# Kernel tuning notes

Hardware: AMD Instinct MI355X
Metric: run time of the kernel (lower is better)

The kernel has to match this reference:

```python
import jax, jax.numpy as jnp
import numpy as np

B, P, F, E, H, V = 128, 196, 2048, 512, 1024, 10000
TMAX = 30  # max(captions_len) - 1 decode steps
BN_EPS = 1e-5


def setup_inputs() -> dict:
    key = jax.random.key(0)
    ks = jax.random.split(key, 14)
    encoder_feat = jax.random.normal(ks[0], (B, P, F), jnp.float32)
    gt_captions = jax.random.randint(ks[1], (B, TMAX + 1), 0, V, dtype=jnp.int32)
    lens = jax.random.randint(ks[2], (B,), 2, TMAX + 2, dtype=jnp.int32)
    lens = lens.at[0].set(TMAX + 1)
    captions_len = jnp.sort(lens)[::-1]  # sorted descending, as the torch slicing assumes
    embedding = jax.random.uniform(ks[3], (V, E), jnp.float32, -0.1, 0.1)
    W_init = jax.random.normal(ks[4], (E, F), jnp.float32) * np.sqrt(2.0 / F)
    b_init = jnp.zeros((E,), jnp.float32)
    bn_gamma = jnp.ones((E,), jnp.float32)
    bn_beta = jnp.zeros((E,), jnp.float32)
    s = 1.0 / np.sqrt(H)
    W_ih = jax.random.uniform(ks[5], (4 * H, E), jnp.float32, -s, s)
    b_ih = jax.random.uniform(ks[6], (4 * H,), jnp.float32, -s, s)
    W_hh = jax.random.uniform(ks[7], (4 * H, H), jnp.float32, -s, s)
    b_hh = jax.random.uniform(ks[8], (4 * H,), jnp.float32, -s, s)
    W_fc = jax.random.normal(ks[9], (V, H), jnp.float32) * np.sqrt(2.0 / H)
    b_fc = jnp.zeros((V,), jnp.float32)
    return {
        'encoder_feat': encoder_feat, 'gt_captions': gt_captions, 'captions_len': captions_len,
        'embedding': embedding, 'W_init': W_init, 'b_init': b_init,
        'bn_gamma': bn_gamma, 'bn_beta': bn_beta,
        'W_ih': W_ih, 'b_ih': b_ih, 'W_hh': W_hh, 'b_hh': b_hh,
        'W_fc': W_fc, 'b_fc': b_fc,
    }


def _lstm_cell(h, c, x, W_ih, b_ih, W_hh, b_hh):
    # PyTorch LSTMCell: gates = x W_ih^T + b_ih + h W_hh^T + b_hh, order [i, f, g, o]
    gates = x @ W_ih.T + b_ih + h @ W_hh.T + b_hh
    i, f, g, o = jnp.split(gates, 4, axis=-1)
    c_new = jax.nn.sigmoid(f) * c + jax.nn.sigmoid(i) * jnp.tanh(g)
    h_new = jax.nn.sigmoid(o) * jnp.tanh(c_new)
    return h_new, c_new


def reference(encoder_feat, gt_captions, captions_len, embedding, W_init, b_init,
              bn_gamma, bn_beta, W_ih, b_ih, W_hh, b_hh, W_fc, b_fc):
    batch = encoder_feat.shape[0]
    hidden = W_hh.shape[1]
    # t == 0: image feature -> sigmoid(linear) -> BatchNorm1d (eval: rm=0, rv=1)
    feat = encoder_feat.mean(axis=1)                      # [B, F]
    x0 = jax.nn.sigmoid(feat @ W_init.T + b_init)         # [B, E]
    x0 = bn_gamma * (x0 / jnp.sqrt(1.0 + BN_EPS)) + bn_beta
    h0 = jnp.zeros((batch, hidden), x0.dtype)
    c0 = jnp.zeros((batch, hidden), x0.dtype)
    h, c = _lstm_cell(h0, c0, x0, W_ih, b_ih, W_hh, b_hh)
    # decode steps t = 1..TMAX over ground-truth token embeddings
    emb = embedding[gt_captions[:, :TMAX]]                # [B, T, E]
    xs = jnp.swapaxes(emb, 0, 1)                          # [T, B, E]

    def step(carry, x_t):
        h, c = carry
        h, c = _lstm_cell(h, c, x_t, W_ih, b_ih, W_hh, b_hh)
        preds = h @ W_fc.T + b_fc                         # [B, V]
        return (h, c), preds

    _, preds = jax.lax.scan(step, (h, c), xs)             # [T, B, V]
    preds = jnp.swapaxes(preds, 0, 1)                     # [B, T, V]
    # rows beyond batch_size_t were never written in torch (zeros tensor) -> mask
    mask = jnp.arange(TMAX)[None, :] < (captions_len - 1)[:, None]  # [B, T]
    return jnp.where(mask[:, :, None], preds, 0.0)
```

## Files before the change

### kernel.cpp

```cpp
#include <hip/hip_runtime.h>
#include <math.h>

typedef __bf16 bf16;
typedef __bf16 bf16x8 __attribute__((ext_vector_type(8)));
typedef __bf16 bf16x4 __attribute__((ext_vector_type(4)));
typedef float f32x4 __attribute__((ext_vector_type(4)));

#define MFMA_B16(a,b,c) __builtin_amdgcn_mfma_f32_16x16x32_bf16((a),(b),(c),0,0,0)

constexpr int TMAXc = 30;
constexpr int Bc = 128, Pc = 196, Fc = 2048, Ec = 512, Hc = 1024, Vc = 10000;
constexpr int G4c = 4 * Hc;
constexpr int NSTEP = TMAXc + 1;
constexpr int MALLc = NSTEP * Bc;
constexpr int MOUTc = TMAXc * Bc;
constexpr int NBLK = 256;

__device__ __forceinline__ float fsigm(float x){
  return __fdividef(1.0f, 1.0f + __expf(-x));
}
__device__ __forceinline__ float ftanh(float x){
  return 1.0f - __fdividef(2.0f, __expf(2.0f*x) + 1.0f);
}
__device__ __forceinline__ float sel4(float a, float b, float c, float d, int i){
  float x = (i & 1) ? b : a;
  float y = (i & 1) ? d : c;
  return (i & 2) ? y : x;
}

__device__ __forceinline__ void gll16(const void* g, void* l){
  __builtin_amdgcn_global_load_lds((const __attribute__((address_space(1))) void*)g,
                                   (__attribute__((address_space(3))) void*)l, 16, 0, 0);
}

__device__ __forceinline__ void wt16(bf16* p, bf16x8 v){
  asm volatile("global_store_dwordx4 %0, %1, off sc0 sc1" :: "v"(p), "v"(v) : "memory");
}

__device__ __forceinline__ int aldf(int* f){
  return __hip_atomic_load(f, __ATOMIC_RELAXED, __HIP_MEMORY_SCOPE_AGENT);
}

__device__ __forceinline__ void waitflag(int* f, int tgt){
  long long t0 = __builtin_amdgcn_s_memrealtime();
  while (aldf(f) < tgt) {
    __builtin_amdgcn_s_sleep(1);
    if (__builtin_amdgcn_s_memrealtime() - t0 > 100000) break;
  }
}

__device__ __forceinline__ void waitflags4(int* F, int& f1, int& f2, int& f3){
  long long t0 = __builtin_amdgcn_s_memrealtime();
  for (;;) {
    int f0 = aldf(F + 0);
    f1 = aldf(F + 1);
    f2 = aldf(F + 2);
    f3 = aldf(F + 3);
    if (f0 >= 32) break;
    __builtin_amdgcn_s_sleep(1);
    if (__builtin_amdgcn_s_memrealtime() - t0 > 100000) break;
  }
}


__global__ void mean_kernel(const float* __restrict__ enc, bf16* __restrict__ feat){
  int blk = blockIdx.x, b = blk >> 1, half = blk & 1;
  int f0 = half*1024 + threadIdx.x*4;
  const float* p = enc + (size_t)b*Pc*Fc + f0;
  float4 s = {0.f,0.f,0.f,0.f};
  #pragma unroll 4
  for (int q = 0; q < Pc; ++q) {
    float4 v = *(const float4*)(p + (size_t)q*Fc);
    s.x += v.x; s.y += v.y; s.z += v.z; s.w += v.w;
  }
  const float r = 1.0f/(float)Pc;
  bf16x4 o = { (bf16)(s.x*r), (bf16)(s.y*r), (bf16)(s.z*r), (bf16)(s.w*r) };
  *(bf16x4*)&feat[b*Fc + f0] = o;
}

__global__ void conv_kernel(const float* __restrict__ src, bf16* __restrict__ dst, int n4){
  int i = blockIdx.x*256 + threadIdx.x;
  if (i >= n4) return;
  float4 v = ((const float4*)src)[i];
  bf16x4 o = { (bf16)v.x, (bf16)v.y, (bf16)v.z, (bf16)v.w };
  *(bf16x4*)&dst[i*4] = o;
}

__global__ void permconv_ih(const float* __restrict__ W, bf16* __restrict__ Wp){
  int i = blockIdx.x*256 + threadIdx.x;
  if (i >= G4c*Ec/4) return;
  int i4 = i*4;
  int rp = i4 >> 9, k = i4 & 511;
  int g = rp & 3, j = rp >> 2;
  float4 v = *(const float4*)&W[(size_t)(g*Hc + j)*Ec + k];
  bf16x4 o = { (bf16)v.x, (bf16)v.y, (bf16)v.z, (bf16)v.w };
  *(bf16x4*)&Wp[i4] = o;
}

__global__ void permsplit_hh(const float* __restrict__ W, bf16* __restrict__ Whi, bf16* __restrict__ Wlo){
  int i = blockIdx.x*256 + threadIdx.x;
  if (i >= G4c*Hc/4) return;
  int i4 = i*4;
  int rp = i4 >> 10, k = i4 & 1023;
  int g = rp & 3, j = rp >> 2;
  float4 v = *(const float4*)&W[(size_t)(g*Hc + j)*Hc + k];
  bf16 h0=(bf16)v.x, h1=(bf16)v.y, h2=(bf16)v.z, h3=(bf16)v.w;
  bf16x4 hi = { h0, h1, h2, h3 };
  bf16x4 lo = { (bf16)(v.x-(float)h0), (bf16)(v.y-(float)h1), (bf16)(v.z-(float)h2), (bf16)(v.w-(float)h3) };
  *(bf16x4*)&Whi[i4] = hi;
  *(bf16x4*)&Wlo[i4] = lo;
}

__global__ void split_kernel(const float* __restrict__ W, bf16* __restrict__ Whi, bf16* __restrict__ Wlo, int n4){
  int i = blockIdx.x*256 + threadIdx.x;
  if (i >= n4) return;
  float4 v = ((const float4*)W)[i];
  bf16 h0=(bf16)v.x, h1=(bf16)v.y, h2=(bf16)v.z, h3=(bf16)v.w;
  bf16x4 hi = { h0, h1, h2, h3 };
  bf16x4 lo = { (bf16)(v.x-(float)h0), (bf16)(v.y-(float)h1), (bf16)(v.z-(float)h2), (bf16)(v.w-(float)h3) };
  *(bf16x4*)&Whi[i*4] = hi;
  *(bf16x4*)&Wlo[i*4] = lo;
}

__global__ void bcomb_kernel(const float* __restrict__ bih, const float* __restrict__ bhh, float* __restrict__ bc){
  int i = blockIdx.x*256 + threadIdx.x;
  if (i >= G4c) return;
  int g = i & 3, j = i >> 2;
  bc[i] = bih[g*Hc + j] + bhh[g*Hc + j];
}

__global__ void gather_kernel(const float* __restrict__ emb, const int* __restrict__ gt, bf16* __restrict__ X){
  int idx = blockIdx.x*256 + threadIdx.x;
  if (idx >= MOUTc*(Ec/4)) return;
  int r = idx >> 7, ei = (idx & 127) * 4;
  int s = (r >> 7) + 1, b = r & 127;
  int tok = gt[b*(TMAXc+1) + (s-1)];
  float4 v = *(const float4*)(emb + (size_t)tok*Ec + ei);
  bf16x4 o = { (bf16)v.x, (bf16)v.y, (bf16)v.z, (bf16)v.w };
  *(bf16x4*)&X[(size_t)(s*Bc + b)*Ec + ei] = o;
}

__global__ void build_ridx(const int* __restrict__ lens, int* __restrict__ meta){
  int i = blockIdx.x*256 + threadIdx.x;
  if (i >= MOUTc) return;
  int t = i >> 7, b = i & 127;
  int S = 0, R = 0;
  for (int bb = 0; bb < 128; ++bb) {
    int l = lens[bb] - 1;
    S += (t < l) ? t : l;
    R += l;
  }
  if (i == 0) meta[0] = R;
  if (i >= R) meta[1 + i] = 0;
  if (t < lens[b] - 1) meta[1 + S + b] = i;
}

__global__ void zerofill(const int* __restrict__ lens, float* __restrict__ out){
  int i = blockIdx.x*256 + threadIdx.x;
  if (i >= MOUTc*2500) return;
  int row = i / 2500, c4 = i - row*2500;
  int b = row / TMAXc, t = row - b*TMAXc;
  if (t >= lens[b] - 1) {
    float4 z = {0.f,0.f,0.f,0.f};
    *(float4*)(out + (size_t)row*Vc + c4*4) = z;
  }
}

__global__ __launch_bounds__(256, 2) void initA(
  const bf16* __restrict__ feat, const bf16* __restrict__ Wi, float* __restrict__ part)
{
  __shared__ alignas(16) bf16 sA[128*32], sB[128*32];
  int tid = threadIdx.x, lane = tid & 63, w = tid >> 6, wr = w >> 1, wc = w & 1;
  int nt = blockIdx.x & 3, kc = blockIdx.x >> 2;
  int n0 = nt*128;

  f32x4 acc[4][4] = {};
  for (int kt = kc*256; kt < kc*256 + 256; kt += 32) {
    #pragma unroll
    for (int is = 0; is < 2; ++is) {
      int p = tid*16 + is*4096;
      int r = p >> 6, c = (p & 63) >> 1;
      int ldsoff = w*512 + is*2048;
      gll16(feat + (size_t)r*Fc + kt + c, &sA[ldsoff]);
      gll16(Wi + (size_t)(n0 + r)*Fc + kt + c, &sB[ldsoff]);
    }
    __syncthreads();
    int koff = (lane >> 4) * 8;
    bf16x8 ah[4], bh[4];
    #pragma unroll
    for (int mi = 0; mi < 4; ++mi)
      ah[mi] = *(const bf16x8*)&sA[(wr*64 + mi*16 + (lane & 15))*32 + koff];
    #pragma unroll
    for (int ni = 0; ni < 4; ++ni)
      bh[ni] = *(const bf16x8*)&sB[(wc*64 + ni*16 + (lane & 15))*32 + koff];
    #pragma unroll
    for (int mi = 0; mi < 4; ++mi)
      #pragma unroll
      for (int ni = 0; ni < 4; ++ni)
        acc[mi][ni] = MFMA_B16(ah[mi], bh[ni], acc[mi][ni]);
    __syncthreads();
  }
  #pragma unroll
  for (int mi = 0; mi < 4; ++mi)
    #pragma unroll
    for (int ni = 0; ni < 4; ++ni) {
      int lrow = wr*64 + mi*16 + ((lane >> 4) << 2);
      int col = n0 + wc*64 + ni*16 + (lane & 15);
      #pragma unroll
      for (int j = 0; j < 4; ++j)
        part[((size_t)kc*128 + lrow + j)*512 + col] = acc[mi][ni][j];
    }
}

__global__ void initB(const float* __restrict__ part, const float* __restrict__ binit,
                      const float* __restrict__ gam, const float* __restrict__ bet,
                      bf16* __restrict__ Xall)
{
  int i = blockIdx.x*256 + threadIdx.x;
  if (i >= 128*512) return;
  int col = i & 511;
  float v = 0.f;
  #pragma unroll
  for (int kc = 0; kc < 8; ++kc) v += part[(size_t)kc*128*512 + i];
  const float rbn = rsqrtf(1.0f + 1e-5f);
  v = fsigm(v + binit[col]);
  v = gam[col]*(v*rbn) + bet[col];
  Xall[i] = (bf16)v;
}

template<int EPI, bool SPLIT, bool XSWZ>
__global__ __launch_bounds__(256, 2) void gemm_kernel(
  const bf16* __restrict__ Ahi, const bf16* __restrict__ Alo,
  const bf16* __restrict__ Bhi, const bf16* __restrict__ Blo,
  int M, int N, int K, int mtiles,
  const float* __restrict__ p0,
  bf16* __restrict__ outb, float* __restrict__ outf, const int* __restrict__ meta)
{
  constexpr int BK = 32;
  __shared__ alignas(16) bf16 sAh[128*BK], sBh[128*BK];
  __shared__ alignas(16) bf16 sAl[SPLIT ? 128*BK : 8], sBl[SPLIT ? 128*BK : 8];

  int tid = threadIdx.x;
  int lane = tid & 63, w = tid >> 6, wr = w >> 1, wc = w & 1;
  int bid = blockIdx.x;
  if constexpr (XSWZ) {
    int nwg = gridDim.x, q = nwg >> 3, r = nwg & 7;
    int x = bid & 7, o = bid >> 3;
    bid = (x < r ? x*(q+1) : r*(q+1) + (x-r)*q) + o;
  }
  int nt = bid / mtiles, mt = bid - nt*mtiles;
  int m0 = mt*128, n0 = nt*128;

  int R = M;
  if constexpr (EPI == 2) {
    R = meta[0];
    if (m0 >= R) return;
  }

  int sr = (tid*16) >> 6;
  int gr0, gr1;
  if constexpr (EPI == 2) { gr0 = meta[1 + m0 + sr]; gr1 = meta[1 + m0 + sr + 64]; }
  else                    { gr0 = m0 + sr;           gr1 = m0 + sr + 64; }

  f32x4 acc[4][4] = {};

  for (int kt = 0; kt < K; kt += BK) {
    #pragma unroll
    for (int is = 0; is < 2; ++is) {
      int p = tid*16 + is*4096;
      int r = p >> 6, c = (p & 63) >> 1;
      int ldsoff = w*512 + is*2048;
      int ga = is ? gr1 : gr0;
      gll16(Ahi + (size_t)ga*K + kt + c, &sAh[ldsoff]);
      int rb = n0 + r; rb = rb < N ? rb : N - 1;
      gll16(Bhi + (size_t)rb*K + kt + c, &sBh[ldsoff]);
      if constexpr (SPLIT) {
        gll16(Alo + (size_t)ga*K + kt + c, &sAl[ldsoff]);
        gll16(Blo + (size_t)rb*K + kt + c, &sBl[ldsoff]);
      }
    }
    __syncthreads();

    int koff = (lane >> 4) * 8;
    bf16x8 ah[4], bh[4], al[SPLIT?4:1], bl[SPLIT?4:1];
    #pragma unroll
    for (int mi = 0; mi < 4; ++mi) {
      int rr = wr*64 + mi*16 + (lane & 15);
      ah[mi] = *(const bf16x8*)&sAh[rr*BK + koff];
      if constexpr (SPLIT) al[mi] = *(const bf16x8*)&sAl[rr*BK + koff];
    }
    #pragma unroll
    for (int ni = 0; ni < 4; ++ni) {
      int rr = wc*64 + ni*16 + (lane & 15);
      bh[ni] = *(const bf16x8*)&sBh[rr*BK + koff];
      if constexpr (SPLIT) bl[ni] = *(const bf16x8*)&sBl[rr*BK + koff];
    }
    #pragma unroll
    for (int mi = 0; mi < 4; ++mi)
      #pragma unroll
      for (int ni = 0; ni < 4; ++ni) {
        acc[mi][ni] = MFMA_B16(ah[mi], bh[ni], acc[mi][ni]);
        if constexpr (SPLIT) {
          acc[mi][ni] = MFMA_B16(ah[mi], bl[ni], acc[mi][ni]);
          acc[mi][ni] = MFMA_B16(al[mi], bh[ni], acc[mi][ni]);
        }
      }
    __syncthreads();
  }

  #pragma unroll
  for (int mi = 0; mi < 4; ++mi) {
    #pragma unroll
    for (int ni = 0; ni < 4; ++ni) {
      int lrow = m0 + wr*64 + mi*16 + ((lane >> 4) << 2);
      int col = n0 + wc*64 + ni*16 + (lane & 15);
      #pragma unroll
      for (int j = 0; j < 4; ++j) {
        int rr = lrow + j;
        float v = acc[mi][ni][j];
        if constexpr (EPI == 1) {
          outb[(size_t)rr*G4c + col] = (bf16)(v + p0[col]);
        } else {
          if (rr < R && col < N) {
            int val = meta[1 + rr];
            int t = val >> 7, b = val & 127;
            outf[(size_t)b*(TMAXc*Vc) + (size_t)t*Vc + col] = v + p0[col];
          }
        }
      }
    }
  }
}


__global__ __launch_bounds__(256, 1) void lstm_persist(
  const bf16* __restrict__ Whi, const bf16* __restrict__ Wlo,
  const bf16* __restrict__ Xg,
  bf16* __restrict__ hCh, bf16* __restrict__ hCl,
  bf16* __restrict__ Hh, bf16* __restrict__ Hl,
  const int* __restrict__ lens,
  int* __restrict__ flg)
{
  extern __shared__ char sWc[];
  int tid = threadIdx.x, lane = tid & 63, w = tid >> 6;
  int bid = blockIdx.x;
  int strip = bid >> 1, rh = bid & 1;
  int pc0 = strip * 32;
  int row0 = rh * 64 + w * 16;
  int grp = strip >> 5;
  char* scr = sWc + 131072 + w*512;

  for (int ch = tid; ch < 4096; ch += 256) {
    int p = ch >> 7;
    int k = (ch & 127) * 8;
    int ni = p >> 4, bp = p & 15;
    int ks = k >> 5, kg = (k >> 3) & 3;
    int off = (((ks*2 + ni)*4 + kg)*16 + bp) * 16;
    bf16x8 vh = *(const bf16x8*)&Whi[(size_t)(pc0 + p)*Hc + k];
    bf16x8 vl = *(const bf16x8*)&Wlo[(size_t)(pc0 + p)*Hc + k];
    *(bf16x8*)(sWc + off) = vh;
    *(bf16x8*)(sWc + 65536 + off) = vl;
  }
  __syncthreads();

  int bp = lane & 15;
  int bk = (lane >> 4) << 3;
  int rbase = row0 + ((lane >> 4) << 2);
  int e = lane & 3;
  const char* sWhiB = sWc + lane*16;
  const char* sWloB = sWc + 65536 + lane*16;

  int Lh = lens[rh * 64];
  if (Lh > NSTEP) Lh = NSTEP;
  int lenv = lens[row0 + (lane & 15)] - 1;

  float creg[2] = {0.f, 0.f};
  float xgv[2][4];
  #pragma unroll
  for (int ni = 0; ni < 2; ++ni)
    #pragma unroll
    for (int j = 0; j < 4; ++j)
      xgv[ni][j] = (float)Xg[(size_t)(rbase + j)*G4c + pc0 + ni*16 + bp];

#define GATEQ(g, fg) do { if (s > 0) { \
    if (tid == 0 && (fg) < 32) waitflag(&flg[(s*2 + rh)*4 + (g)], 32); \
    __builtin_amdgcn_s_barrier(); \
    asm volatile("" ::: "memory"); } } while (0)

#define LOADQ(qh, ql, g) do { \
    _Pragma("unroll") \
    for (int i = 0; i < 8; ++i) { \
      qh[i] = *(const bf16x8*)(pah + ((g)*8 + i)*32); \
      ql[i] = *(const bf16x8*)(pal + ((g)*8 + i)*32); \
    } \
    asm volatile("" ::: "memory"); } while (0)

#define MFMAQ(qh, ql, g) do { \
    _Pragma("unroll") \
    for (int i = 0; i < 8; ++i) { \
      int ks = (g)*8 + i; \
      _Pragma("unroll") \
      for (int ni = 0; ni < 2; ++ni) { \
        bf16x8 bvh = *(const bf16x8*)(sWhiB + (ks*2 + ni)*1024); \
        bf16x8 bvl = *(const bf16x8*)(sWloB + (ks*2 + ni)*1024); \
        aHH[ni] = MFMA_B16(qh[i], bvh, aHH[ni]); \
        aHL[ni] = MFMA_B16(qh[i], bvl, aHL[ni]); \
        aLH[ni] = MFMA_B16(ql[i], bvh, aLH[ni]); \
      } \
    } } while (0)

  #pragma unroll 1
  for (int s = 0; s < Lh; ++s) {
    const bf16* pah = hCh + (size_t)s*Bc*Hc + (size_t)(row0 + bp)*Hc + bk;
    const bf16* pal = hCl + (size_t)s*Bc*Hc + (size_t)(row0 + bp)*Hc + bk;
    bf16* hwh = hCh + (size_t)(s+1)*Bc*Hc;
    bf16* hwl = hCl + (size_t)(s+1)*Bc*Hc;

    f32x4 aHH[2], aHL[2], aLH[2];
    #pragma unroll
    for (int ni = 0; ni < 2; ++ni) {
      #pragma unroll
      for (int j = 0; j < 4; ++j) aHH[ni][j] = xgv[ni][j];
      aHL[ni] = (f32x4){0.f,0.f,0.f,0.f};
      aLH[ni] = (f32x4){0.f,0.f,0.f,0.f};
    }

    bf16x8 qh0[8], ql0[8], qh1[8], ql1[8];
    int f1 = 32, f2 = 32, f3 = 32;

    if (s > 0) {
      if (tid == 0) waitflags4(&flg[(s*2 + rh)*4], f1, f2, f3);
      __builtin_amdgcn_s_barrier();
      asm volatile("" ::: "memory");
    }
    LOADQ(qh0, ql0, 0);
    GATEQ(1, f1); LOADQ(qh1, ql1, 1);
    MFMAQ(qh0, ql0, 0);
    GATEQ(2, f2); LOADQ(qh0, ql0, 2);
    MFMAQ(qh1, ql1, 1);
    GATEQ(3, f3); LOADQ(qh1, ql1, 3);
    MFMAQ(qh0, ql0, 2);
    MFMAQ(qh1, ql1, 3);

    #pragma unroll
    for (int ni = 0; ni < 2; ++ni) {
      float v0 = aHH[ni][0] + aHL[ni][0] + aLH[ni][0];
      float v1 = aHH[ni][1] + aHL[ni][1] + aLH[ni][1];
      float v2 = aHH[ni][2] + aHL[ni][2] + aLH[ni][2];
      float v3 = aHH[ni][3] + aHL[ni][3] + aLH[ni][3];
      float g0 = sel4(v0, v1, v2, v3, e);
      float g1 = __shfl_xor(sel4(v0, v1, v2, v3, e ^ 1), 1);
      float g2 = __shfl_xor(sel4(v0, v1, v2, v3, e ^ 2), 2);
      float g3 = __shfl_xor(sel4(v0, v1, v2, v3, e ^ 3), 3);
      float gI = sel4(g0, g1, g2, g3, e);
      float gF = sel4(g0, g1, g2, g3, e ^ 1);
      float gG = sel4(g0, g1, g2, g3, e ^ 2);
      float gO = sel4(g0, g1, g2, g3, e ^ 3);

      float co = creg[ni];
      float cn = fsigm(gF)*co + fsigm(gI)*ftanh(gG);
      float hn = fsigm(gO)*ftanh(cn);
      creg[ni] = cn;
      bf16 hhi = (bf16)hn;
      int r16 = ((lane >> 4) << 2) + e;
      int c8  = ni*4 + (bp >> 2);
      *(bf16*)(scr + (r16*8 + c8)*2) = hhi;
      *(bf16*)(scr + 256 + (r16*8 + c8)*2) = (bf16)(hn - (float)hhi);
    }

    asm volatile("s_waitcnt lgkmcnt(0)" ::: "memory");
    __builtin_amdgcn_sched_barrier(0);

    if (lane < 32) {
      int r = lane & 15, buf = lane >> 4;
      bf16x8 vv = *(const bf16x8*)(scr + buf*256 + r*16);
      bf16* dst = (buf ? hwl : hwh) + (size_t)(row0 + r)*Hc + strip*8;
      wt16(dst, vv);
    }

    __syncthreads();
    if (tid == 0 && s + 1 < Lh)
      __hip_atomic_fetch_add(&flg[((s+1)*2 + rh)*4 + grp], 1,
                             __ATOMIC_RELAXED, __HIP_MEMORY_SCOPE_AGENT);

    if (s > 0 && lane >= 32 && (s - 1) < lenv) {
      int r = lane & 15, buf = (lane >> 4) & 1;
      bf16x8 vv = *(const bf16x8*)(scr + buf*256 + r*16);
      *(bf16x8*)((buf ? Hl : Hh) + (size_t)((s-1)*Bc + row0 + r)*Hc + strip*8) = vv;
    }
    if (s + 1 < Lh) {
      #pragma unroll
      for (int ni = 0; ni < 2; ++ni)
        #pragma unroll
        for (int j = 0; j < 4; ++j)
          xgv[ni][j] = (float)Xg[(size_t)((s+1)*Bc + rbase + j)*G4c + pc0 + ni*16 + bp];
    }
  }
#undef GATEQ
#undef LOADQ
#undef MFMAQ
}


extern "C" void kernel_launch(void* const* d_in, const int* in_sizes, int n_in,
                              void* d_out, int out_size, void* d_ws, size_t ws_size,
                              hipStream_t stream)
{
  const float* enc   = (const float*)d_in[0];
  const int*   gt    = (const int*)  d_in[1];
  const int*   lens  = (const int*)  d_in[2];
  const float* emb   = (const float*)d_in[3];
  const float* Winit = (const float*)d_in[4];
  const float* binit = (const float*)d_in[5];
  const float* gam   = (const float*)d_in[6];
  const float* bet   = (const float*)d_in[7];
  const float* Wih   = (const float*)d_in[8];
  const float* bih   = (const float*)d_in[9];
  const float* Whh   = (const float*)d_in[10];
  const float* bhh   = (const float*)d_in[11];
  const float* Wfc   = (const float*)d_in[12];
  const float* bfc   = (const float*)d_in[13];
  float* out = (float*)d_out;

  char* ws = (char*)d_ws;
  size_t off = 0;
  auto alloc = [&](size_t bytes) -> char* {
    char* p = ws + off;
    off += (bytes + 255) & ~(size_t)255;
    return p;
  };

  bf16* featB  = (bf16*)alloc((size_t)Bc*Fc*2);
  bf16* WinitB = (bf16*)alloc((size_t)Ec*Fc*2);
  bf16* WihpB  = (bf16*)alloc((size_t)G4c*Ec*2);
  bf16* WhhHi  = (bf16*)alloc((size_t)G4c*Hc*2);
  bf16* WhhLo  = (bf16*)alloc((size_t)G4c*Hc*2);
  bf16* WfcHi  = (bf16*)alloc((size_t)Vc*Hc*2);
  bf16* WfcLo  = (bf16*)alloc((size_t)Vc*Hc*2);
  float* bcomb = (float*)alloc((size_t)G4c*4);
  bf16* Xall   = (bf16*)alloc((size_t)MALLc*Ec*2);
  bf16* Xg     = (bf16*)alloc((size_t)MALLc*G4c*2);
  bf16* hChH   = (bf16*)alloc((size_t)(NSTEP+1)*Bc*Hc*2);
  bf16* hChL   = (bf16*)alloc((size_t)(NSTEP+1)*Bc*Hc*2);
  bf16* HallH  = (bf16*)alloc((size_t)MOUTc*Hc*2);
  bf16* HallL  = (bf16*)alloc((size_t)MOUTc*Hc*2);
  float* part  = (float*)alloc((size_t)8*128*512*4);
  int*  meta   = (int*) alloc((size_t)(1 + MOUTc)*4);
  int*  flg    = (int*) alloc((size_t)256*4);

  if (off > ws_size) return;

  hipMemsetAsync(hChH, 0, (size_t)Bc*Hc*2, stream);
  hipMemsetAsync(hChL, 0, (size_t)Bc*Hc*2, stream);
  hipMemsetAsync(flg, 0, (size_t)256*4, stream);

  mean_kernel<<<256, 256, 0, stream>>>(enc, featB);
  conv_kernel<<<(Ec*Fc/4 + 255)/256, 256, 0, stream>>>(Winit, WinitB, Ec*Fc/4);
  permconv_ih<<<(G4c*Ec/4 + 255)/256, 256, 0, stream>>>(Wih, WihpB);
  permsplit_hh<<<(G4c*Hc/4 + 255)/256, 256, 0, stream>>>(Whh, WhhHi, WhhLo);
  split_kernel<<<(Vc*Hc/4 + 255)/256, 256, 0, stream>>>(Wfc, WfcHi, WfcLo, Vc*Hc/4);
  bcomb_kernel<<<(G4c + 255)/256, 256, 0, stream>>>(bih, bhh, bcomb);
  gather_kernel<<<(MOUTc*(Ec/4) + 255)/256, 256, 0, stream>>>(emb, gt, Xall);
  build_ridx<<<(MOUTc + 255)/256, 256, 0, stream>>>(lens, meta);
  zerofill<<<(MOUTc*2500 + 255)/256, 256, 0, stream>>>(lens, out);

  initA<<<32, 256, 0, stream>>>(featB, WinitB, part);
  initB<<<(128*512 + 255)/256, 256, 0, stream>>>(part, binit, gam, bet, Xall);

  gemm_kernel<1,false,true><<<31*32, 256, 0, stream>>>(
      Xall, nullptr, WihpB, nullptr, MALLc, G4c, Ec, 31,
      bcomb, Xg, nullptr, nullptr);

  hipFuncSetAttribute(reinterpret_cast<const void*>(lstm_persist),
                      hipFuncAttributeMaxDynamicSharedMemorySize, 133120);
  lstm_persist<<<NBLK, 256, 133120, stream>>>(
      WhhHi, WhhLo, Xg, hChH, hChL, HallH, HallL, lens, flg);

  gemm_kernel<2,true,true><<<79*30, 256, 0, stream>>>(
      HallH, HallL, WfcHi, WfcLo, MOUTc, Vc, Hc, 30,
      bfc, nullptr, out, meta);
}
```

Measured before the change: 646.0 us.

## Fuse output FC GEMM into persistent LSTM kernel with per-step readiness flags

Removes the separate output-projection GEMM launch and runs it inside the persistent LSTM kernel. Blocks that finish their recurrence take FC tiles from a global atomic work queue, and each tile waits on per-timestep counters that signal its hidden states are written. This lets the large FC GEMM overlap the sequential LSTM tail and fill idle CUs, and it adds double-buffered LDS staging to the FC loop. The cost is extra atomics and spin-waits, hidden-state writes changed to write-through, and a block count capped at 256 for the FC work.

```diff
diff --git a/kernel.cpp b/kernel.cpp
--- a/kernel.cpp
+++ b/kernel.cpp
@@ -228,22 +228,18 @@
   Xall[i] = (bf16)v;
 }
 
-template<int EPI, bool SPLIT, bool XSWZ>
-__global__ __launch_bounds__(256, 2) void gemm_kernel(
-  const bf16* __restrict__ Ahi, const bf16* __restrict__ Alo,
-  const bf16* __restrict__ Bhi, const bf16* __restrict__ Blo,
+__global__ __launch_bounds__(256, 2) void gemm_xg(
+  const bf16* __restrict__ A, const bf16* __restrict__ B,
   int M, int N, int K, int mtiles,
-  const float* __restrict__ p0,
-  bf16* __restrict__ outb, float* __restrict__ outf, const int* __restrict__ meta)
+  const float* __restrict__ p0, bf16* __restrict__ outb)
 {
   constexpr int BK = 32;
   __shared__ alignas(16) bf16 sAh[128*BK], sBh[128*BK];
-  __shared__ alignas(16) bf16 sAl[SPLIT ? 128*BK : 8], sBl[SPLIT ? 128*BK : 8];
 
   int tid = threadIdx.x;
   int lane = tid & 63, w = tid >> 6, wr = w >> 1, wc = w & 1;
   int bid = blockIdx.x;
-  if constexpr (XSWZ) {
+  {
     int nwg = gridDim.x, q = nwg >> 3, r = nwg & 7;
     int x = bid & 7, o = bid >> 3;
     bid = (x < r ? x*(q+1) : r*(q+1) + (x-r)*q) + o;
@@ -251,16 +247,8 @@
   int nt = bid / mtiles, mt = bid - nt*mtiles;
   int m0 = mt*128, n0 = nt*128;
 
-  int R = M;
-  if constexpr (EPI == 2) {
-    R = meta[0];
-    if (m0 >= R) return;
-  }
-
   int sr = (tid*16) >> 6;
-  int gr0, gr1;
-  if constexpr (EPI == 2) { gr0 = meta[1 + m0 + sr]; gr1 = meta[1 + m0 + sr + 64]; }
-  else                    { gr0 = m0 + sr;           gr1 = m0 + sr + 64; }
+  int gr0 = m0 + sr, gr1 = m0 + sr + 64;
 
   f32x4 acc[4][4] = {};
 
@@ -268,68 +256,41 @@
     #pragma unroll
     for (int is = 0; is < 2; ++is) {
       int p = tid*16 + is*4096;
-      int r = p >> 6, c = (p & 63) >> 1;
+      int c = (p & 63) >> 1;
+      int r = p >> 6;
       int ldsoff = w*512 + is*2048;
       int ga = is ? gr1 : gr0;
-      gll16(Ahi + (size_t)ga*K + kt + c, &sAh[ldsoff]);
-      int rb = n0 + r; rb = rb < N ? rb : N - 1;
-      gll16(Bhi + (size_t)rb*K + kt + c, &sBh[ldsoff]);
-      if constexpr (SPLIT) {
-        gll16(Alo + (size_t)ga*K + kt + c, &sAl[ldsoff]);
-        gll16(Blo + (size_t)rb*K + kt + c, &sBl[ldsoff]);
-      }
+      gll16(A + (size_t)ga*K + kt + c, &sAh[ldsoff]);
+      gll16(B + (size_t)(n0 + r)*K + kt + c, &sBh[ldsoff]);
     }
     __syncthreads();
 
     int koff = (lane >> 4) * 8;
-    bf16x8 ah[4], bh[4], al[SPLIT?4:1], bl[SPLIT?4:1];
-    #pragma unroll
-    for (int mi = 0; mi < 4; ++mi) {
-      int rr = wr*64 + mi*16 + (lane & 15);
-      ah[mi] = *(const bf16x8*)&sAh[rr*BK + koff];
-      if constexpr (SPLIT) al[mi] = *(const bf16x8*)&sAl[rr*BK + koff];
-    }
-    #pragma unroll
-    for (int ni = 0; ni < 4; ++ni) {
-      int rr = wc*64 + ni*16 + (lane & 15);
-      bh[ni] = *(const bf16x8*)&sBh[rr*BK + koff];
-      if constexpr (SPLIT) bl[ni] = *(const bf16x8*)&sBl[rr*BK + koff];
-    }
+    bf16x8 ah[4], bh[4];
     #pragma unroll
     for (int mi = 0; mi < 4; ++mi)
-      #pragma unroll
-      for (int ni = 0; ni < 4; ++ni) {
+      ah[mi] = *(const bf16x8*)&sAh[(wr*64 + mi*16 + (lane & 15))*BK + koff];
+    #pragma unroll
+    for (int ni = 0; ni < 4; ++ni)
+      bh[ni] = *(const bf16x8*)&sBh[(wc*64 + ni*16 + (lane & 15))*BK + koff];
+    #pragma unroll
+    for (int mi = 0; mi < 4; ++mi)
+      #pragma unroll
+      for (int ni = 0; ni < 4; ++ni)
         acc[mi][ni] = MFMA_B16(ah[mi], bh[ni], acc[mi][ni]);
-        if constexpr (SPLIT) {
-          acc[mi][ni] = MFMA_B16(ah[mi], bl[ni], acc[mi][ni]);
-          acc[mi][ni] = MFMA_B16(al[mi], bh[ni], acc[mi][ni]);
-        }
-      }
     __syncthreads();
   }
 
   #pragma unroll
-  for (int mi = 0; mi < 4; ++mi) {
+  for (int mi = 0; mi < 4; ++mi)
     #pragma unroll
     for (int ni = 0; ni < 4; ++ni) {
       int lrow = m0 + wr*64 + mi*16 + ((lane >> 4) << 2);
       int col = n0 + wc*64 + ni*16 + (lane & 15);
       #pragma unroll
-      for (int j = 0; j < 4; ++j) {
-        int rr = lrow + j;
-        float v = acc[mi][ni][j];
-        if constexpr (EPI == 1) {
-          outb[(size_t)rr*G4c + col] = (bf16)(v + p0[col]);
-        } else {
-          if (rr < R && col < N) {
-            int val = meta[1 + rr];
-            int t = val >> 7, b = val & 127;
-            outf[(size_t)b*(TMAXc*Vc) + (size_t)t*Vc + col] = v + p0[col];
-          }
-        }
-      }
-    }
-  }
+      for (int j = 0; j < 4; ++j)
+        outb[(size_t)(lrow + j)*G4c + col] = (bf16)(acc[mi][ni][j] + p0[col]);
+    }
 }
 
 
@@ -338,7 +299,10 @@
   const bf16* __restrict__ Xg,
   bf16* __restrict__ hCh, bf16* __restrict__ hCl,
   bf16* __restrict__ Hh, bf16* __restrict__ Hl,
-  const int* __restrict__ lens,
+  const bf16* __restrict__ WfcHi, const bf16* __restrict__ WfcLo,
+  const float* __restrict__ bfc,
+  const int* __restrict__ lens, const int* __restrict__ meta,
+  float* __restrict__ outf,
   int* __restrict__ flg)
 {
   extern __shared__ char sWc[];
@@ -349,6 +313,8 @@
   int row0 = rh * 64 + w * 16;
   int grp = strip >> 5;
   char* scr = sWc + 131072 + w*512;
+  int* hallflg = flg + 256;
+  int* tilectr = flg + 320;
 
   for (int ch = tid; ch < 4096; ch += 256) {
     int p = ch >> 7;
@@ -486,7 +452,7 @@
     if (s > 0 && lane >= 32 && (s - 1) < lenv) {
       int r = lane & 15, buf = (lane >> 4) & 1;
       bf16x8 vv = *(const bf16x8*)(scr + buf*256 + r*16);
-      *(bf16x8*)((buf ? Hl : Hh) + (size_t)((s-1)*Bc + row0 + r)*Hc + strip*8) = vv;
+      wt16((buf ? Hl : Hh) + (size_t)((s-1)*Bc + row0 + r)*Hc + strip*8, vv);
     }
     if (s + 1 < Lh) {
       #pragma unroll
@@ -495,10 +461,130 @@
         for (int j = 0; j < 4; ++j)
           xgv[ni][j] = (float)Xg[(size_t)((s+1)*Bc + rbase + j)*G4c + pc0 + ni*16 + bp];
     }
+
+    __syncthreads();
+    if (tid == 0 && s > 0)
+      __hip_atomic_fetch_add(&hallflg[(s-1)*2 + rh], 1,
+                             __ATOMIC_RELAXED, __HIP_MEMORY_SCOPE_AGENT);
   }
 #undef GATEQ
 #undef LOADQ
 #undef MFMAQ
+
+  if (tid == 0)
+    for (int t = Lh - 1; t < TMAXc; ++t)
+      __hip_atomic_fetch_add(&hallflg[t*2 + rh], 1,
+                             __ATOMIC_RELAXED, __HIP_MEMORY_SCOPE_AGENT);
+
+  __syncthreads();
+
+  bf16* sAh2 = (bf16*)(sWc);
+  bf16* sBh2 = (bf16*)(sWc + 32768);
+  bf16* sAl2 = (bf16*)(sWc + 65536);
+  bf16* sBl2 = (bf16*)(sWc + 98304);
+  int* ctrl  = (int*)(sWc + 131072 + 2044);
+
+  int R = meta[0];
+  int mtilesFC = (R + 127) >> 7;
+  int ntFC = mtilesFC * 79;
+  int wr = w >> 1, wc2 = w & 1;
+
+#define STAGE_FC(buf, kt) do { \
+    _Pragma("unroll") \
+    for (int is = 0; is < 2; ++is) { \
+      int p = tid*16 + is*4096; \
+      int c = (p & 63) >> 1; \
+      int r = p >> 6; \
+      int ldsoff = (buf)*4096 + w*512 + is*2048; \
+      int ga = is ? gr1 : gr0; \
+      int rb = n0 + r; if (rb > 9999) rb = 9999; \
+      gll16(Hh + (size_t)ga*Hc + (kt) + c, &sAh2[ldsoff]); \
+      gll16(WfcHi + (size_t)rb*Hc + (kt) + c, &sBh2[ldsoff]); \
+      gll16(Hl + (size_t)ga*Hc + (kt) + c, &sAl2[ldsoff]); \
+      gll16(WfcLo + (size_t)rb*Hc + (kt) + c, &sBl2[ldsoff]); \
+    } } while (0)
+
+  #pragma unroll 1
+  for (;;) {
+    if (tid == 0) ctrl[0] = __hip_atomic_fetch_add(tilectr, 1,
+                               __ATOMIC_RELAXED, __HIP_MEMORY_SCOPE_AGENT);
+    __syncthreads();
+    int idx = ctrl[0];
+    __syncthreads();
+    if (idx >= ntFC) break;
+    int mt = idx / 79, ntc = idx - mt*79;
+    int m0 = mt*128, n0 = ntc*128;
+    int last = m0 + 127; if (last >= R) last = R - 1;
+    int tmax = meta[1 + last] >> 7;
+    if (tid == 0) {
+      waitflag(&hallflg[tmax*2 + 0], 128);
+      waitflag(&hallflg[tmax*2 + 1], 128);
+    }
+    __builtin_amdgcn_s_barrier();
+    asm volatile("" ::: "memory");
+
+    int sr = (tid*16) >> 6;
+    int gr0 = meta[1 + m0 + sr], gr1 = meta[1 + m0 + sr + 64];
+
+    f32x4 acc[4][4] = {};
+
+    STAGE_FC(0, 0);
+    asm volatile("s_waitcnt vmcnt(0)" ::: "memory");
+    __builtin_amdgcn_s_barrier();
+    asm volatile("" ::: "memory");
+
+    #pragma unroll 1
+    for (int ks = 0; ks < 32; ++ks) {
+      int buf = ks & 1;
+      if (ks + 1 < 32) STAGE_FC(buf ^ 1, (ks+1)*32);
+
+      int koff = (lane >> 4) * 8;
+      int bb = buf*4096;
+      bf16x8 ah[4], bh[4], al[4], bl[4];
+      #pragma unroll
+      for (int mi = 0; mi < 4; ++mi) {
+        int rr = wr*64 + mi*16 + (lane & 15);
+        ah[mi] = *(const bf16x8*)&sAh2[bb + rr*32 + koff];
+        al[mi] = *(const bf16x8*)&sAl2[bb + rr*32 + koff];
+      }
+      #pragma unroll
+      for (int ni = 0; ni < 4; ++ni) {
+        int rr = wc2*64 + ni*16 + (lane & 15);
+        bh[ni] = *(const bf16x8*)&sBh2[bb + rr*32 + koff];
+        bl[ni] = *(const bf16x8*)&sBl2[bb + rr*32 + koff];
+      }
+      #pragma unroll
+      for (int mi = 0; mi < 4; ++mi)
+        #pragma unroll
+        for (int ni = 0; ni < 4; ++ni) {
+          acc[mi][ni] = MFMA_B16(ah[mi], bh[ni], acc[mi][ni]);
+          acc[mi][ni] = MFMA_B16(ah[mi], bl[ni], acc[mi][ni]);
+          acc[mi][ni] = MFMA_B16(al[mi], bh[ni], acc[mi][ni]);
+        }
+
+      asm volatile("s_waitcnt vmcnt(0)" ::: "memory");
+      __builtin_amdgcn_s_barrier();
+      asm volatile("" ::: "memory");
+    }
+
+    #pragma unroll
+    for (int mi = 0; mi < 4; ++mi)
+      #pragma unroll
+      for (int ni = 0; ni < 4; ++ni) {
+        int lrow = m0 + wr*64 + mi*16 + ((lane >> 4) << 2);
+        int col = n0 + wc2*64 + ni*16 + (lane & 15);
+        #pragma unroll
+        for (int j = 0; j < 4; ++j) {
+          int rr = lrow + j;
+          if (rr < R && col < Vc) {
+            int val = meta[1 + rr];
+            int t = val >> 7, b = val & 127;
+            outf[(size_t)b*(TMAXc*Vc) + (size_t)t*Vc + col] = acc[mi][ni][j] + bfc[col];
+          }
+        }
+      }
+  }
+#undef STAGE_FC
 }
 
 
@@ -546,13 +632,13 @@
   bf16* HallL  = (bf16*)alloc((size_t)MOUTc*Hc*2);
   float* part  = (float*)alloc((size_t)8*128*512*4);
   int*  meta   = (int*) alloc((size_t)(1 + MOUTc)*4);
-  int*  flg    = (int*) alloc((size_t)256*4);
+  int*  flg    = (int*) alloc((size_t)384*4);
 
   if (off > ws_size) return;
 
   hipMemsetAsync(hChH, 0, (size_t)Bc*Hc*2, stream);
   hipMemsetAsync(hChL, 0, (size_t)Bc*Hc*2, stream);
-  hipMemsetAsync(flg, 0, (size_t)256*4, stream);
+  hipMemsetAsync(flg, 0, (size_t)384*4, stream);
 
   mean_kernel<<<256, 256, 0, stream>>>(enc, featB);
   conv_kernel<<<(Ec*Fc/4 + 255)/256, 256, 0, stream>>>(Winit, WinitB, Ec*Fc/4);
@@ -567,16 +653,12 @@
   initA<<<32, 256, 0, stream>>>(featB, WinitB, part);
   initB<<<(128*512 + 255)/256, 256, 0, stream>>>(part, binit, gam, bet, Xall);
 
-  gemm_kernel<1,false,true><<<31*32, 256, 0, stream>>>(
-      Xall, nullptr, WihpB, nullptr, MALLc, G4c, Ec, 31,
-      bcomb, Xg, nullptr, nullptr);
+  gemm_xg<<<31*32, 256, 0, stream>>>(
+      Xall, WihpB, MALLc, G4c, Ec, 31, bcomb, Xg);
 
   hipFuncSetAttribute(reinterpret_cast<const void*>(lstm_persist),
                       hipFuncAttributeMaxDynamicSharedMemorySize, 133120);
   lstm_persist<<<NBLK, 256, 133120, stream>>>(
-      WhhHi, WhhLo, Xg, hChH, hChL, HallH, HallL, lens, flg);
-
-  gemm_kernel<2,true,true><<<79*30, 256, 0, stream>>>(
-      HallH, HallL, WfcHi, WfcLo, MOUTc, Vc, Hc, 30,
-      bfc, nullptr, out, meta);
-}
+      WhhHi, WhhLo, Xg, hChH, hChL, HallH, HallL,
+      WfcHi, WfcLo, bfc, lens, meta, out, flg);
+}
```

Result: no change. 653.0 us (+1.1%).
